# Performance work log

Hardware: AMD Instinct MI355X
Metric: run time of the kernel (lower is better)

## Reference

```python
import jax, jax.numpy as jnp
import numpy as np

N_NODES = 250000
N_EDGES = 8000000
F_IN = 16
N_GRAPHS = 512
BN_EPS = 1e-5


def setup_inputs() -> dict:
    key = jax.random.key(0)
    ks = jax.random.split(key, 16)
    x = jax.random.normal(ks[0], (N_NODES, F_IN), dtype=jnp.float32)
    edge_index = jax.random.randint(ks[1], (2, N_EDGES), 0, N_NODES, dtype=jnp.int64)
    batch = jnp.sort(jax.random.randint(ks[2], (N_NODES,), 0, N_GRAPHS, dtype=jnp.int64))
    def lin(k, fan_in, fan_out):
        s = 1.0 / np.sqrt(fan_in)
        kw, kb = jax.random.split(k)
        W = jax.random.uniform(kw, (fan_in, fan_out), jnp.float32, -s, s)
        b = jax.random.uniform(kb, (fan_out,), jnp.float32, -s, s)
        return W, b
    W1a, b1a = lin(ks[3], F_IN, 32)
    W1b, b1b = lin(ks[4], 32, 16)
    W2a, b2a = lin(ks[5], 16, 16)
    W2b, b2b = lin(ks[6], 16, 16)
    Wfc, bfc = lin(ks[7], 32, 2)
    return {
        'x': x,
        'W1a': W1a, 'b1a': b1a, 'W1b': W1b, 'b1b': b1b,
        'g1': jnp.ones((16,), jnp.float32), 'be1': jnp.zeros((16,), jnp.float32),
        'W2a': W2a, 'b2a': b2a, 'W2b': W2b, 'b2b': b2b,
        'g2': jnp.ones((16,), jnp.float32), 'be2': jnp.zeros((16,), jnp.float32),
        'Wfc': Wfc, 'bfc': bfc,
        'edge_index': edge_index, 'batch': batch,
    }


def _mlp(h, Wa, ba, Wb, bb):
    # Linear -> ReLU -> (Dropout=identity in eval) -> Linear -> ReLU
    h = jax.nn.relu(h @ Wa + ba)
    return jax.nn.relu(h @ Wb + bb)


def _bn(h, gamma, beta):
    # BatchNorm1d over node axis, training-mode batch statistics, biased var
    mean = jnp.mean(h, axis=0)
    var = jnp.mean(jnp.square(h - mean), axis=0)
    return gamma * (h - mean) * jax.lax.rsqrt(var + BN_EPS) + beta


def _gin_conv(h, src, dst, Wa, ba, Wb, bb):
    # GINConv, eps=0: nn((1+eps)*h + sum_{j in N(i)} h_j)
    agg = jax.ops.segment_sum(h[src], dst, num_segments=N_NODES)
    return _mlp(h + agg, Wa, ba, Wb, bb)


def reference(x, W1a, b1a, W1b, b1b, g1, be1, W2a, b2a, W2b, b2b, g2, be2, Wfc, bfc, edge_index, batch):
    src, dst = edge_index[0], edge_index[1]
    h = jax.nn.relu(_bn(_gin_conv(x, src, dst, W1a, b1a, W1b, b1b), g1, be1))
    h = jax.nn.relu(_bn(_gin_conv(h, src, dst, W2a, b2a, W2b, b2b), g2, be2))
    # global max / mean pool over graphs
    x_max = jax.ops.segment_max(h, batch, num_segments=N_GRAPHS)
    x_max = jnp.where(jnp.isfinite(x_max), x_max, 0.0)  # guard empty segments
    counts = jax.ops.segment_sum(jnp.ones((h.shape[0], 1), h.dtype), batch, num_segments=N_GRAPHS)
    x_mean = jax.ops.segment_sum(h, batch, num_segments=N_GRAPHS) / jnp.maximum(counts, 1.0)
    pooled = jnp.concatenate([x_max, x_mean], axis=1)  # [G, 32]
    return pooled @ Wfc + bfc
```

## Files before the change

kernel.cpp:

```cpp
#include <hip/hip_runtime.h>

#define F 16
#define N_GRAPHS_C 512
#define BN_EPS 1e-5f

#define NBSHIFT 8
#define BSZ (1 << NBSHIFT)
#define MAXB 1024
#define SRCBITS 18
#define SRCMASK ((1u << SRCBITS) - 1u)
#define PCHUNK 8192
#define CAP 8960
#define CAPB 9216

__device__ inline unsigned short f2bf(float f) {
    unsigned u = __float_as_uint(f);
    return (unsigned short)((u + 0x7fffu + ((u >> 16) & 1u)) >> 16);
}

__global__ __launch_bounds__(256) void k_scatter(
    const float* __restrict__ h, const int* __restrict__ src,
    const int* __restrict__ dst, float* __restrict__ agg, int n_edges)
{
    int idx = blockIdx.x * 256 + threadIdx.x;
    int tot = n_edges << 2;
    if (idx >= tot) return;
    int e = idx >> 2, q = idx & 3;
    int s = src[e], d = dst[e];
    float4 v = reinterpret_cast<const float4*>(h + (size_t)s * F)[q];
    float* o = agg + (size_t)d * F + q * 4;
    atomicAdd(o + 0, v.x);
    atomicAdd(o + 1, v.y);
    atomicAdd(o + 2, v.z);
    atomicAdd(o + 3, v.w);
}

__global__ __launch_bounds__(256) void k_tobf16(
    const float* __restrict__ in, unsigned short* __restrict__ out, int n4)
{
    int i = blockIdx.x * 256 + threadIdx.x;
    if (i >= n4) return;
    float4 v = reinterpret_cast<const float4*>(in)[i];
    ushort4 o;
    o.x = f2bf(v.x); o.y = f2bf(v.y); o.z = f2bf(v.z); o.w = f2bf(v.w);
    reinterpret_cast<ushort4*>(out)[i] = o;
}

__global__ __launch_bounds__(256) void k_partition(
    const int* __restrict__ src, const int* __restrict__ dst, int n_edges,
    unsigned* __restrict__ gcur, unsigned* __restrict__ part, int nbk)
{
    __shared__ unsigned hist[MAXB];
    __shared__ unsigned offs[MAXB + 1];
    __shared__ unsigned lcur[MAXB];
    __shared__ unsigned gbase[MAXB];
    __shared__ unsigned stage[PCHUNK];

    int base = blockIdx.x * PCHUNK;
    int cnt = n_edges - base; if (cnt > PCHUNK) cnt = PCHUNK;
    if (cnt <= 0) return;

    for (int i = threadIdx.x; i < nbk; i += 256) hist[i] = 0;
    __syncthreads();
    for (int i = threadIdx.x; i < cnt; i += 256)
        atomicAdd(&hist[dst[base + i] >> NBSHIFT], 1u);
    __syncthreads();
    if (threadIdx.x == 0) {
        unsigned run = 0;
        for (int b = 0; b < nbk; b++) { offs[b] = run; run += hist[b]; }
        offs[nbk] = run;
    }
    __syncthreads();
    for (int b = threadIdx.x; b < nbk; b += 256) {
        lcur[b] = offs[b];
        unsigned hb = hist[b];
        gbase[b] = hb ? ((unsigned)b * CAPB + atomicAdd(&gcur[b], hb)) : 0u;
    }
    __syncthreads();
    for (int i = threadIdx.x; i < cnt; i += 256) {
        int d = dst[base + i];
        int b = d >> NBSHIFT;
        unsigned p = (unsigned)src[base + i] | (((unsigned)d & (BSZ - 1u)) << SRCBITS);
        stage[atomicAdd(&lcur[b], 1u)] = p;
    }
    __syncthreads();
    for (int i = threadIdx.x; i < cnt; i += 256) {
        int lo = 0, hi = nbk;
        while (hi - lo > 1) { int m = (lo + hi) >> 1; if (offs[m] <= (unsigned)i) lo = m; else hi = m; }
        part[gbase[lo] + ((unsigned)i - offs[lo])] = stage[i];
    }
}

__global__ __launch_bounds__(256, 4) void k_aggregate(
    const unsigned short* __restrict__ hb, const unsigned* __restrict__ part,
    const unsigned* __restrict__ gcur, float* __restrict__ agg, int n_nodes)
{
    __shared__ unsigned stage[CAP];
    __shared__ unsigned hist[BSZ];
    __shared__ unsigned offs[BSZ];
    __shared__ unsigned cursor[BSZ];
    __shared__ unsigned wsum[4];

    const int b = blockIdx.x;
    const unsigned s = (unsigned)b * CAPB;
    const unsigned e = s + gcur[b];
    const int t = threadIdx.x;
    const int lane = t & 63, w = t >> 6;

    float acc[F];
#pragma unroll
    for (int k = 0; k < F; k++) acc[k] = 0.f;

#define ACC8(U, B0) \
    acc[B0+0] += __uint_as_float((U).x << 16); \
    acc[B0+1] += __uint_as_float((U).x & 0xffff0000u); \
    acc[B0+2] += __uint_as_float((U).y << 16); \
    acc[B0+3] += __uint_as_float((U).y & 0xffff0000u); \
    acc[B0+4] += __uint_as_float((U).z << 16); \
    acc[B0+5] += __uint_as_float((U).z & 0xffff0000u); \
    acc[B0+6] += __uint_as_float((U).w << 16); \
    acc[B0+7] += __uint_as_float((U).w & 0xffff0000u);

    for (unsigned base = s; base < e; base += CAP) {
        unsigned cnt = e - base; if (cnt > CAP) cnt = CAP;

        hist[t] = 0;
        __syncthreads();
        for (unsigned i = t; i < cnt; i += 256)
            atomicAdd(&hist[part[base + i] >> SRCBITS], 1u);
        __syncthreads();
        unsigned hv = hist[t];
        unsigned inc = hv;
#pragma unroll
        for (int d = 1; d < 64; d <<= 1) {
            unsigned up = __shfl_up(inc, d);
            if (lane >= d) inc += up;
        }
        if (lane == 63) wsum[w] = inc;
        __syncthreads();
        unsigned wo = 0;
        for (int ww = 0; ww < w; ww++) wo += wsum[ww];
        unsigned excl = wo + inc - hv;
        offs[t] = excl;
        cursor[t] = excl;
        __syncthreads();
        for (unsigned i = t; i < cnt; i += 256) {
            unsigned p = part[base + i];
            unsigned pos = atomicAdd(&cursor[p >> SRCBITS], 1u);
            stage[pos] = p & SRCMASK;
        }
        __syncthreads();
        unsigned k = offs[t];
        const unsigned kend = cursor[t];
        if (k < kend) {
            unsigned srcA = stage[k];
            const uint4* hpA = reinterpret_cast<const uint4*>(hb + (size_t)srcA * F);
            uint4 a0 = hpA[0], a1 = hpA[1];
            for (++k; k < kend; ++k) {
                unsigned srcB = stage[k];
                const uint4* hpB = reinterpret_cast<const uint4*>(hb + (size_t)srcB * F);
                uint4 b0 = hpB[0], b1 = hpB[1];
                ACC8(a0, 0) ACC8(a1, 8)
                a0 = b0; a1 = b1;
            }
            ACC8(a0, 0) ACC8(a1, 8)
        }
        __syncthreads();
    }
#undef ACC8

    int r = (b << NBSHIFT) + t;
    if (r < n_nodes) {
        float4* op = reinterpret_cast<float4*>(agg + (size_t)r * F);
        op[0] = make_float4(acc[0],  acc[1],  acc[2],  acc[3]);
        op[1] = make_float4(acc[4],  acc[5],  acc[6],  acc[7]);
        op[2] = make_float4(acc[8],  acc[9],  acc[10], acc[11]);
        op[3] = make_float4(acc[12], acc[13], acc[14], acc[15]);
    }
}

template <int HID, bool BF>
__global__ __launch_bounds__(256) void k_mlp_stats(
    const void* __restrict__ xin, const float* agg,
    const float* __restrict__ Wa, const float* __restrict__ ba,
    const float* __restrict__ Wb, const float* __restrict__ bb,
    float* hpre, float* __restrict__ stats, int n_nodes)
{
    __shared__ float sWa[F * HID], sba[HID], sWb[HID * F], sbb[F];
    for (int i = threadIdx.x; i < F * HID; i += 256) sWa[i] = Wa[i];
    for (int i = threadIdx.x; i < HID * F; i += 256) sWb[i] = Wb[i];
    if (threadIdx.x < HID) sba[threadIdx.x] = ba[threadIdx.x];
    if (threadIdx.x < F)   sbb[threadIdx.x] = bb[threadIdx.x];
    __syncthreads();

    int node = blockIdx.x * 256 + threadIdx.x;
    float o[F];
    if (node < n_nodes) {
        float v[F];
        if (BF) {
            const uint4* xp = reinterpret_cast<const uint4*>(
                (const unsigned short*)xin + (size_t)node * F);
            uint4 u0 = xp[0], u1 = xp[1];
            v[0]  = __uint_as_float(u0.x << 16); v[1]  = __uint_as_float(u0.x & 0xffff0000u);
            v[2]  = __uint_as_float(u0.y << 16); v[3]  = __uint_as_float(u0.y & 0xffff0000u);
            v[4]  = __uint_as_float(u0.z << 16); v[5]  = __uint_as_float(u0.z & 0xffff0000u);
            v[6]  = __uint_as_float(u0.w << 16); v[7]  = __uint_as_float(u0.w & 0xffff0000u);
            v[8]  = __uint_as_float(u1.x << 16); v[9]  = __uint_as_float(u1.x & 0xffff0000u);
            v[10] = __uint_as_float(u1.y << 16); v[11] = __uint_as_float(u1.y & 0xffff0000u);
            v[12] = __uint_as_float(u1.z << 16); v[13] = __uint_as_float(u1.z & 0xffff0000u);
            v[14] = __uint_as_float(u1.w << 16); v[15] = __uint_as_float(u1.w & 0xffff0000u);
        } else {
            const float4* xp = reinterpret_cast<const float4*>(
                (const float*)xin + (size_t)node * F);
#pragma unroll
            for (int q = 0; q < 4; q++) {
                float4 a = xp[q];
                v[q * 4 + 0] = a.x; v[q * 4 + 1] = a.y;
                v[q * 4 + 2] = a.z; v[q * 4 + 3] = a.w;
            }
        }
        const float4* ap = reinterpret_cast<const float4*>(agg + (size_t)node * F);
#pragma unroll
        for (int q = 0; q < 4; q++) {
            float4 bq = ap[q];
            v[q * 4 + 0] += bq.x; v[q * 4 + 1] += bq.y;
            v[q * 4 + 2] += bq.z; v[q * 4 + 3] += bq.w;
        }
        float hid[HID];
#pragma unroll
        for (int j = 0; j < HID; j++) hid[j] = sba[j];
#pragma unroll
        for (int k = 0; k < F; k++) {
            float vk = v[k];
#pragma unroll
            for (int j = 0; j < HID; j++) hid[j] = fmaf(vk, sWa[k * HID + j], hid[j]);
        }
#pragma unroll
        for (int j = 0; j < HID; j++) hid[j] = fmaxf(hid[j], 0.f);
#pragma unroll
        for (int j = 0; j < F; j++) o[j] = sbb[j];
#pragma unroll
        for (int k = 0; k < HID; k++) {
            float hk = hid[k];
#pragma unroll
            for (int j = 0; j < F; j++) o[j] = fmaf(hk, sWb[k * F + j], o[j]);
        }
#pragma unroll
        for (int j = 0; j < F; j++) o[j] = fmaxf(o[j], 0.f);
        float4* op = reinterpret_cast<float4*>(hpre + (size_t)node * F);
        op[0] = make_float4(o[0], o[1], o[2], o[3]);
        op[1] = make_float4(o[4], o[5], o[6], o[7]);
        op[2] = make_float4(o[8], o[9], o[10], o[11]);
        op[3] = make_float4(o[12], o[13], o[14], o[15]);
    } else {
#pragma unroll
        for (int j = 0; j < F; j++) o[j] = 0.f;
    }

    __shared__ float red[4][2 * F];
    int lane = threadIdx.x & 63, wid = threadIdx.x >> 6;
#pragma unroll
    for (int j = 0; j < F; j++) {
        float s = o[j], ss = o[j] * o[j];
#pragma unroll
        for (int off = 32; off; off >>= 1) {
            s  += __shfl_down(s, off);
            ss += __shfl_down(ss, off);
        }
        if (lane == 0) { red[wid][j] = s; red[wid][F + j] = ss; }
    }
    __syncthreads();
    if (threadIdx.x < 2 * F) {
        float t = red[0][threadIdx.x] + red[1][threadIdx.x] +
                  red[2][threadIdx.x] + red[3][threadIdx.x];
        atomicAdd(&stats[threadIdx.x], t);
    }
}

template <bool BFOUT>
__global__ __launch_bounds__(256) void k_bn_relu(
    const float* __restrict__ hpre, const float* __restrict__ stats,
    const float* __restrict__ gamma, const float* __restrict__ beta,
    void* __restrict__ hout, int n_nodes)
{
    int idx = blockIdx.x * 256 + threadIdx.x;
    int tot = n_nodes * 4;
    if (idx >= tot) return;
    int q = idx & 3;
    float4 v = reinterpret_cast<const float4*>(hpre)[idx];
    float invN = 1.f / (float)n_nodes;
    float r[4];
    float vin[4] = {v.x, v.y, v.z, v.w};
#pragma unroll
    for (int t = 0; t < 4; t++) {
        int j = q * 4 + t;
        float mean = stats[j] * invN;
        float var  = stats[F + j] * invN - mean * mean;
        float sc   = gamma[j] * rsqrtf(var + BN_EPS);
        r[t] = fmaxf((vin[t] - mean) * sc + beta[j], 0.f);
    }
    if (BFOUT) {
        ushort4 o;
        o.x = f2bf(r[0]); o.y = f2bf(r[1]); o.z = f2bf(r[2]); o.w = f2bf(r[3]);
        reinterpret_cast<ushort4*>(hout)[idx] = o;
    } else {
        reinterpret_cast<float4*>(hout)[idx] = make_float4(r[0], r[1], r[2], r[3]);
    }
}

template <bool BFIN>
__global__ __launch_bounds__(256) void k_pool_fc(
    const void* __restrict__ h, const int* __restrict__ batch,
    const float* __restrict__ Wfc, const float* __restrict__ bfc,
    float* __restrict__ out, int n_nodes)
{
    int g = blockIdx.x;
    int lo = 0, hi = n_nodes;
    while (lo < hi) { int m = (lo + hi) >> 1; if (batch[m] < g) lo = m + 1; else hi = m; }
    int start = lo;
    hi = n_nodes;
    while (lo < hi) { int m = (lo + hi) >> 1; if (batch[m] < g + 1) lo = m + 1; else hi = m; }
    int end = lo;

    float mx[F], sm[F];
#pragma unroll
    for (int j = 0; j < F; j++) { mx[j] = 0.f; sm[j] = 0.f; }

    for (int i = start + (int)threadIdx.x; i < end; i += 256) {
        float v[F];
        if (BFIN) {
            const uint4* p = reinterpret_cast<const uint4*>(
                (const unsigned short*)h + (size_t)i * F);
            uint4 u0 = p[0], u1 = p[1];
            v[0]  = __uint_as_float(u0.x << 16); v[1]  = __uint_as_float(u0.x & 0xffff0000u);
            v[2]  = __uint_as_float(u0.y << 16); v[3]  = __uint_as_float(u0.y & 0xffff0000u);
            v[4]  = __uint_as_float(u0.z << 16); v[5]  = __uint_as_float(u0.z & 0xffff0000u);
            v[6]  = __uint_as_float(u0.w << 16); v[7]  = __uint_as_float(u0.w & 0xffff0000u);
            v[8]  = __uint_as_float(u1.x << 16); v[9]  = __uint_as_float(u1.x & 0xffff0000u);
            v[10] = __uint_as_float(u1.y << 16); v[11] = __uint_as_float(u1.y & 0xffff0000u);
            v[12] = __uint_as_float(u1.z << 16); v[13] = __uint_as_float(u1.z & 0xffff0000u);
            v[14] = __uint_as_float(u1.w << 16); v[15] = __uint_as_float(u1.w & 0xffff0000u);
        } else {
            const float4* p = reinterpret_cast<const float4*>(
                (const float*)h + (size_t)i * F);
#pragma unroll
            for (int q = 0; q < 4; q++) {
                float4 vv = p[q];
                v[q * 4 + 0] = vv.x; v[q * 4 + 1] = vv.y;
                v[q * 4 + 2] = vv.z; v[q * 4 + 3] = vv.w;
            }
        }
#pragma unroll
        for (int j = 0; j < F; j++) { mx[j] = fmaxf(mx[j], v[j]); sm[j] += v[j]; }
    }
#pragma unroll
    for (int j = 0; j < F; j++) {
#pragma unroll
        for (int off = 32; off; off >>= 1) {
            mx[j] = fmaxf(mx[j], __shfl_down(mx[j], off));
            sm[j] += __shfl_down(sm[j], off);
        }
    }
    __shared__ float rmx[4][F], rsm[4][F];
    int lane = threadIdx.x & 63, wid = threadIdx.x >> 6;
    if (lane == 0) {
#pragma unroll
        for (int j = 0; j < F; j++) { rmx[wid][j] = mx[j]; rsm[wid][j] = sm[j]; }
    }
    __syncthreads();
    if (threadIdx.x == 0) {
        float pooled[2 * F];
        int cnt = end - start;
        float inv = 1.f / (float)(cnt > 0 ? cnt : 1);
#pragma unroll
        for (int j = 0; j < F; j++) {
            float m = fmaxf(fmaxf(rmx[0][j], rmx[1][j]), fmaxf(rmx[2][j], rmx[3][j]));
            float s = rsm[0][j] + rsm[1][j] + rsm[2][j] + rsm[3][j];
            pooled[j]     = m;
            pooled[F + j] = s * inv;
        }
#pragma unroll
        for (int c = 0; c < 2; c++) {
            float acc = bfc[c];
#pragma unroll
            for (int k = 0; k < 2 * F; k++) acc = fmaf(pooled[k], Wfc[k * 2 + c], acc);
            out[g * 2 + c] = acc;
        }
    }
}

extern "C" void kernel_launch(void* const* d_in, const int* in_sizes, int n_in,
                              void* d_out, int out_size, void* d_ws, size_t ws_size,
                              hipStream_t stream) {
    const float* x    = (const float*)d_in[0];
    const float* W1a  = (const float*)d_in[1];
    const float* b1a  = (const float*)d_in[2];
    const float* W1b  = (const float*)d_in[3];
    const float* b1b  = (const float*)d_in[4];
    const float* g1   = (const float*)d_in[5];
    const float* be1  = (const float*)d_in[6];
    const float* W2a  = (const float*)d_in[7];
    const float* b2a  = (const float*)d_in[8];
    const float* W2b  = (const float*)d_in[9];
    const float* b2b  = (const float*)d_in[10];
    const float* g2   = (const float*)d_in[11];
    const float* be2  = (const float*)d_in[12];
    const float* Wfc  = (const float*)d_in[13];
    const float* bfc  = (const float*)d_in[14];
    const int*   eidx = (const int*)d_in[15];
    const int*   batch= (const int*)d_in[16];

    const int n_nodes = in_sizes[0] / F;
    const int n_edges = in_sizes[15] / 2;
    const int* src = eidx;
    const int* dst = eidx + n_edges;

    const size_t NBf = (size_t)n_nodes * F * sizeof(float);
    const size_t NBh = (size_t)n_nodes * F * sizeof(unsigned short);
    const int nbk = (n_nodes + BSZ - 1) >> NBSHIFT;
    float* out = (float*)d_out;

    const int nblk_nodes = (n_nodes + 255) / 256;
    const int nblk_el4   = (n_nodes * 4 + 255) / 256;

    size_t off = 0;
    auto take = [&](size_t bytes) { size_t o = off; off = (off + bytes + 255) & ~(size_t)255; return o; };
    size_t meta_bytes = (size_t)(nbk + 64) * sizeof(unsigned);
    size_t meta_off = take(meta_bytes);
    size_t part_off = take((size_t)nbk * CAPB * sizeof(unsigned));
    size_t agg_off  = take(NBf);
    size_t tbf_off  = take(NBh);
    bool fast = (nbk <= MAXB) && (n_nodes <= (1 << SRCBITS)) && (off <= ws_size);

    char* ws = (char*)d_ws;
    if (fast) {
        unsigned* meta    = (unsigned*)(ws + meta_off);
        unsigned* gcur    = meta;
        float*    stats1  = (float*)(meta + nbk);
        float*    stats2  = stats1 + 32;
        unsigned* part    = (unsigned*)(ws + part_off);
        float*    agg     = (float*)(ws + agg_off);
        unsigned short* tbf = (unsigned short*)(ws + tbf_off);

        hipMemsetAsync(meta, 0, meta_bytes, stream);
        int npart = (n_edges + PCHUNK - 1) / PCHUNK;
        k_partition<<<npart, 256, 0, stream>>>(src, dst, n_edges, gcur, part, nbk);
        k_tobf16<<<nblk_el4, 256, 0, stream>>>(x, tbf, n_nodes * 4);

        k_aggregate<<<nbk, 256, 0, stream>>>(tbf, part, gcur, agg, n_nodes);
        k_mlp_stats<32, false><<<nblk_nodes, 256, 0, stream>>>(x, agg, W1a, b1a, W1b, b1b,
                                                               agg , stats1, n_nodes);
        k_bn_relu<true><<<nblk_el4, 256, 0, stream>>>(agg, stats1, g1, be1, tbf, n_nodes);

        k_aggregate<<<nbk, 256, 0, stream>>>(tbf, part, gcur, agg, n_nodes);
        k_mlp_stats<16, true><<<nblk_nodes, 256, 0, stream>>>(tbf, agg, W2a, b2a, W2b, b2b,
                                                              agg , stats2, n_nodes);
        k_bn_relu<true><<<nblk_el4, 256, 0, stream>>>(agg, stats2, g2, be2, tbf, n_nodes);

        k_pool_fc<true><<<N_GRAPHS_C, 256, 0, stream>>>(tbf, batch, Wfc, bfc, out, n_nodes);
    } else {
        float* hpre = (float*)(ws);
        float* hbuf = (float*)(ws + NBf);
        float* agg  = (float*)(ws + 2 * NBf);
        float* stats= (float*)(ws + 3 * NBf);
        const int nblk_edges = (int)(((long long)n_edges * 4 + 255) / 256);

        hipMemsetAsync(agg, 0, NBf, stream);
        hipMemsetAsync(stats, 0, 2 * F * sizeof(float), stream);
        k_scatter<<<nblk_edges, 256, 0, stream>>>(x, src, dst, agg, n_edges);
        k_mlp_stats<32, false><<<nblk_nodes, 256, 0, stream>>>(x, agg, W1a, b1a, W1b, b1b,
                                                               hpre, stats, n_nodes);
        k_bn_relu<false><<<nblk_el4, 256, 0, stream>>>(hpre, stats, g1, be1, hbuf, n_nodes);

        hipMemsetAsync(agg, 0, NBf, stream);
        hipMemsetAsync(stats, 0, 2 * F * sizeof(float), stream);
        k_scatter<<<nblk_edges, 256, 0, stream>>>(hbuf, src, dst, agg, n_edges);
        k_mlp_stats<16, false><<<nblk_nodes, 256, 0, stream>>>(hbuf, agg, W2a, b2a, W2b, b2b,
                                                               hpre, stats, n_nodes);
        k_bn_relu<false><<<nblk_el4, 256, 0, stream>>>(hpre, stats, g2, be2, hbuf, n_nodes);

        k_pool_fc<false><<<N_GRAPHS_C, 256, 0, stream>>>(hbuf, batch, Wfc, bfc, out, n_nodes);
    }
}
```

Baseline: 550.8 us.

## Fuse bf16 conversion into partition kernel, parallelize scan, unroll gather by four

Merges the x-to-bf16 conversion into the edge partition launch as extra grid-stride blocks, removing one kernel launch and letting the two independent jobs run at the same time. Replaces the serial single-thread prefix sum over bucket histograms with a wave-shuffle scan. Unrolls the per-node gather loop in the aggregate kernel to issue four neighbor row loads at once for more memory-level parallelism, at the cost of more registers.

```diff
diff --git a/kernel.cpp b/kernel.cpp
--- a/kernel.cpp
+++ b/kernel.cpp
@@ -35,56 +35,80 @@
     atomicAdd(o + 3, v.w);
 }
 
-__global__ __launch_bounds__(256) void k_tobf16(
-    const float* __restrict__ in, unsigned short* __restrict__ out, int n4)
+__global__ __launch_bounds__(256) void k_partition_conv(
+    const int* __restrict__ src, const int* __restrict__ dst, int n_edges,
+    unsigned* __restrict__ gcur, unsigned* __restrict__ part, int nbk,
+    const float* __restrict__ xf, unsigned short* __restrict__ tbf, int n4,
+    int npart)
 {
-    int i = blockIdx.x * 256 + threadIdx.x;
-    if (i >= n4) return;
-    float4 v = reinterpret_cast<const float4*>(in)[i];
-    ushort4 o;
-    o.x = f2bf(v.x); o.y = f2bf(v.y); o.z = f2bf(v.z); o.w = f2bf(v.w);
-    reinterpret_cast<ushort4*>(out)[i] = o;
-}
-
-__global__ __launch_bounds__(256) void k_partition(
-    const int* __restrict__ src, const int* __restrict__ dst, int n_edges,
-    unsigned* __restrict__ gcur, unsigned* __restrict__ part, int nbk)
-{
+    if ((int)blockIdx.x >= npart) {
+        int nb = (int)gridDim.x - npart;
+        for (int i = ((int)blockIdx.x - npart) * 256 + (int)threadIdx.x;
+             i < n4; i += nb * 256) {
+            float4 v = reinterpret_cast<const float4*>(xf)[i];
+            ushort4 o;
+            o.x = f2bf(v.x); o.y = f2bf(v.y); o.z = f2bf(v.z); o.w = f2bf(v.w);
+            reinterpret_cast<ushort4*>(tbf)[i] = o;
+        }
+        return;
+    }
+
     __shared__ unsigned hist[MAXB];
     __shared__ unsigned offs[MAXB + 1];
     __shared__ unsigned lcur[MAXB];
     __shared__ unsigned gbase[MAXB];
     __shared__ unsigned stage[PCHUNK];
+    __shared__ unsigned wsum[4];
+
+    const int t = threadIdx.x;
+    const int lane = t & 63, w = t >> 6;
 
     int base = blockIdx.x * PCHUNK;
     int cnt = n_edges - base; if (cnt > PCHUNK) cnt = PCHUNK;
     if (cnt <= 0) return;
 
-    for (int i = threadIdx.x; i < nbk; i += 256) hist[i] = 0;
-    __syncthreads();
-    for (int i = threadIdx.x; i < cnt; i += 256)
+    for (int i = t; i < nbk; i += 256) hist[i] = 0;
+    __syncthreads();
+    for (int i = t; i < cnt; i += 256)
         atomicAdd(&hist[dst[base + i] >> NBSHIFT], 1u);
     __syncthreads();
-    if (threadIdx.x == 0) {
-        unsigned run = 0;
-        for (int b = 0; b < nbk; b++) { offs[b] = run; run += hist[b]; }
-        offs[nbk] = run;
-    }
-    __syncthreads();
-    for (int b = threadIdx.x; b < nbk; b += 256) {
+    int t4 = t * 4;
+    unsigned h0 = (t4 + 0 < nbk) ? hist[t4 + 0] : 0u;
+    unsigned h1 = (t4 + 1 < nbk) ? hist[t4 + 1] : 0u;
+    unsigned h2 = (t4 + 2 < nbk) ? hist[t4 + 2] : 0u;
+    unsigned h3 = (t4 + 3 < nbk) ? hist[t4 + 3] : 0u;
+    unsigned tsum = h0 + h1 + h2 + h3;
+    unsigned incl = tsum;
+#pragma unroll
+    for (int d = 1; d < 64; d <<= 1) {
+        unsigned u = __shfl_up(incl, d);
+        if (lane >= d) incl += u;
+    }
+    if (lane == 63) wsum[w] = incl;
+    __syncthreads();
+    unsigned wo = 0;
+    for (int ww = 0; ww < w; ww++) wo += wsum[ww];
+    unsigned ex = wo + incl - tsum;
+    if (t4 + 0 < nbk) offs[t4 + 0] = ex;
+    if (t4 + 1 < nbk) offs[t4 + 1] = ex + h0;
+    if (t4 + 2 < nbk) offs[t4 + 2] = ex + h0 + h1;
+    if (t4 + 3 < nbk) offs[t4 + 3] = ex + h0 + h1 + h2;
+    if (t == 0) offs[nbk] = (unsigned)cnt;
+    __syncthreads();
+    for (int b = t; b < nbk; b += 256) {
         lcur[b] = offs[b];
         unsigned hb = hist[b];
         gbase[b] = hb ? ((unsigned)b * CAPB + atomicAdd(&gcur[b], hb)) : 0u;
     }
     __syncthreads();
-    for (int i = threadIdx.x; i < cnt; i += 256) {
+    for (int i = t; i < cnt; i += 256) {
         int d = dst[base + i];
         int b = d >> NBSHIFT;
         unsigned p = (unsigned)src[base + i] | (((unsigned)d & (BSZ - 1u)) << SRCBITS);
         stage[atomicAdd(&lcur[b], 1u)] = p;
     }
     __syncthreads();
-    for (int i = threadIdx.x; i < cnt; i += 256) {
+    for (int i = t; i < cnt; i += 256) {
         int lo = 0, hi = nbk;
         while (hi - lo > 1) { int m = (lo + hi) >> 1; if (offs[m] <= (unsigned)i) lo = m; else hi = m; }
         part[gbase[lo] + ((unsigned)i - offs[lo])] = stage[i];
@@ -152,18 +176,28 @@
         __syncthreads();
         unsigned k = offs[t];
         const unsigned kend = cursor[t];
-        if (k < kend) {
-            unsigned srcA = stage[k];
-            const uint4* hpA = reinterpret_cast<const uint4*>(hb + (size_t)srcA * F);
-            uint4 a0 = hpA[0], a1 = hpA[1];
-            for (++k; k < kend; ++k) {
-                unsigned srcB = stage[k];
-                const uint4* hpB = reinterpret_cast<const uint4*>(hb + (size_t)srcB * F);
-                uint4 b0 = hpB[0], b1 = hpB[1];
-                ACC8(a0, 0) ACC8(a1, 8)
-                a0 = b0; a1 = b1;
-            }
-            ACC8(a0, 0) ACC8(a1, 8)
+        while (k + 4 <= kend) {
+            unsigned s0 = stage[k + 0], s1 = stage[k + 1];
+            unsigned s2 = stage[k + 2], s3 = stage[k + 3];
+            const uint4* p0 = reinterpret_cast<const uint4*>(hb + (size_t)s0 * F);
+            const uint4* p1 = reinterpret_cast<const uint4*>(hb + (size_t)s1 * F);
+            const uint4* p2 = reinterpret_cast<const uint4*>(hb + (size_t)s2 * F);
+            const uint4* p3 = reinterpret_cast<const uint4*>(hb + (size_t)s3 * F);
+            uint4 a0 = p0[0], b0 = p0[1];
+            uint4 a1 = p1[0], b1 = p1[1];
+            uint4 a2 = p2[0], b2 = p2[1];
+            uint4 a3 = p3[0], b3 = p3[1];
+            ACC8(a0, 0) ACC8(b0, 8)
+            ACC8(a1, 0) ACC8(b1, 8)
+            ACC8(a2, 0) ACC8(b2, 8)
+            ACC8(a3, 0) ACC8(b3, 8)
+            k += 4;
+        }
+        for (; k < kend; ++k) {
+            unsigned s0 = stage[k];
+            const uint4* p0 = reinterpret_cast<const uint4*>(hb + (size_t)s0 * F);
+            uint4 a0 = p0[0], b0 = p0[1];
+            ACC8(a0, 0) ACC8(b0, 8)
         }
         __syncthreads();
     }
@@ -444,8 +478,9 @@
 
         hipMemsetAsync(meta, 0, meta_bytes, stream);
         int npart = (n_edges + PCHUNK - 1) / PCHUNK;
-        k_partition<<<npart, 256, 0, stream>>>(src, dst, n_edges, gcur, part, nbk);
-        k_tobf16<<<nblk_el4, 256, 0, stream>>>(x, tbf, n_nodes * 4);
+        int nconv = nbk;
+        k_partition_conv<<<npart + nconv, 256, 0, stream>>>(
+            src, dst, n_edges, gcur, part, nbk, x, tbf, n_nodes * 4, npart);
 
         k_aggregate<<<nbk, 256, 0, stream>>>(tbf, part, gcur, agg, n_nodes);
         k_mlp_stats<32, false><<<nblk_nodes, 256, 0, stream>>>(x, agg, W1a, b1a, W1b, b1b,
```

After: 533.8 us. 1.03x faster.
